# Optimization experiments

Hardware: AMD Instinct MI355X
Metric: run time of the kernel (lower is better)

The kernel has to match this reference:

```python
import jax, jax.numpy as jnp
import numpy as np

N_NODES = 100000
N_EDGES = 1000000
N_INPUT = 64
N_HIDDEN = 64
K = 8


def setup_inputs() -> dict:
    key = jax.random.key(0)
    k1, k2, k3, k4 = jax.random.split(key, 4)
    x = jax.random.normal(k1, (N_NODES, N_INPUT), dtype=jnp.float32)
    edge_index = jax.random.randint(k2, (2, N_EDGES), 0, N_NODES, dtype=jnp.int64)
    # ChebConv has K independent [in, out] weight matrices (Glorot-ish scale) and a bias.
    weight = jax.random.normal(k3, (K, N_INPUT, N_HIDDEN), dtype=jnp.float32) * (1.0 / np.sqrt(N_INPUT))
    bias = jax.random.normal(k4, (N_HIDDEN,), dtype=jnp.float32) * 0.01
    return {"x": x, "edge_index": edge_index, "weight": weight, "bias": bias}


def _cheb_edge_norm(edge_index, num_nodes):
    # PyG ChebConv sym normalization with default lambda_max=2.0:
    #   L_hat = (2/lambda_max) * (I - D^-1/2 A D^-1/2) - I = -D^-1/2 A D^-1/2
    # (the diagonal +1 from the Laplacian and the -1 self-loop cancel exactly).
    src, dst = edge_index[0], edge_index[1]
    ones = jnp.ones(src.shape[0], dtype=jnp.float32)
    deg = jax.ops.segment_sum(ones, src, num_segments=num_nodes)
    deg_inv_sqrt = jnp.where(deg > 0, jax.lax.rsqrt(jnp.maximum(deg, 1.0)), 0.0)
    return -deg_inv_sqrt[src] * deg_inv_sqrt[dst]  # [E]


def reference(x, edge_index, weight, bias):
    num_nodes = x.shape[0]
    src, dst = edge_index[0], edge_index[1]
    norm = _cheb_edge_norm(edge_index, num_nodes)

    def prop(h):  # h: [N, F] -> L_hat @ h via gather-multiply-scatter over edges
        return jax.ops.segment_sum(norm[:, None] * h[src], dst, num_segments=num_nodes)

    # Chebyshev recursion: T0 = x, T1 = L_hat x, Tk = 2 L_hat T_{k-1} - T_{k-2}
    Tx0 = x
    out = Tx0 @ weight[0]
    Tx1 = prop(Tx0)
    out = out + Tx1 @ weight[1]
    for k in range(2, weight.shape[0]):
        Tx2 = 2.0 * prop(Tx1) - Tx0
        out = out + Tx2 @ weight[k]
        Tx0, Tx1 = Tx1, Tx2
    out = out + bias
    # bn=False path: ReLU then dropout (identity in eval mode)
    return jax.nn.relu(out)
```

## Files before the change

kernel.cpp:

```cpp
#include <hip/hip_runtime.h>
#include <hip/hip_bf16.h>

typedef __attribute__((ext_vector_type(8))) short s16x8;
typedef __attribute__((ext_vector_type(4))) float f32x4;

#define HC 48
#define RBH 6400
#define RBS 3200

static __device__ __forceinline__ unsigned short f2bf(float f) {
    unsigned int u = __float_as_uint(f);
    unsigned int r = (u + 0x7FFFu + ((u >> 16) & 1u)) >> 16;
    return (unsigned short)r;
}

__global__ __launch_bounds__(256) void k_hist(const int* __restrict__ eidx,
                                              unsigned short* __restrict__ partials,
                                              int N, int E, int HR) {
    __shared__ int h[RBH];
    int b = blockIdx.x;
    int job = b / (HR * HC);
    int rc = b % (HR * HC);
    int r = rc / HC, c = rc % HC;
    int lo = r * RBH;
    int nb = min(RBH, N - lo);
    if (nb <= 0) return;
    for (int i = threadIdx.x; i < nb; i += 256) h[i] = 0;
    __syncthreads();
    const int* vals = eidx + (size_t)job * E;
    int e0 = (int)(((long long)E * c / HC) & ~3LL);
    int e1 = (c == HC - 1) ? E : (int)(((long long)E * (c + 1) / HC) & ~3LL);
    int e = e0 + threadIdx.x * 4;
    for (; e + 4 <= e1; e += 1024) {
        int4 v = *reinterpret_cast<const int4*>(vals + e);
        unsigned r0 = (unsigned)(v.x - lo), r1 = (unsigned)(v.y - lo);
        unsigned r2 = (unsigned)(v.z - lo), r3 = (unsigned)(v.w - lo);
        if (r0 < (unsigned)nb) atomicAdd(&h[r0], 1);
        if (r1 < (unsigned)nb) atomicAdd(&h[r1], 1);
        if (r2 < (unsigned)nb) atomicAdd(&h[r2], 1);
        if (r3 < (unsigned)nb) atomicAdd(&h[r3], 1);
    }
    if (threadIdx.x == 0)
        for (int t = e1 & ~3; t < e1; ++t) {
            unsigned rel = (unsigned)(vals[t] - lo);
            if (rel < (unsigned)nb) atomicAdd(&h[rel], 1);
        }
    __syncthreads();
    unsigned short* outp = partials + ((size_t)(job * HC + c)) * N + lo;
    for (int i = threadIdx.x; i < nb; i += 256) outp[i] = (unsigned short)h[i];
}

__global__ void k_reduce(const unsigned short* __restrict__ partials,
                         float* __restrict__ dis, int* __restrict__ cnt, int N) {
    int n = blockIdx.x * blockDim.x + threadIdx.x;
    if (n >= N) return;
    int dsum = 0, csum = 0;
    for (int c = 0; c < HC; ++c) {
        dsum += partials[(size_t)c * N + n];
        csum += partials[(size_t)(HC + c) * N + n];
    }
    dis[n] = dsum > 0 ? rsqrtf((float)dsum) : 0.f;
    cnt[n] = csum;
}

__global__ void k_scan1(const int* __restrict__ cnt, int* __restrict__ incl,
                        int* __restrict__ bsum, int N) {
    __shared__ int sm[1024];
    int t = threadIdx.x;
    int i = blockIdx.x * 1024 + t;
    sm[t] = (i < N) ? cnt[i] : 0;
    __syncthreads();
    for (int off = 1; off < 1024; off <<= 1) {
        int add = (t >= off) ? sm[t - off] : 0;
        __syncthreads();
        sm[t] += add;
        __syncthreads();
    }
    if (i < N) incl[i] = sm[t];
    if (t == 1023) bsum[blockIdx.x] = sm[1023];
}

__global__ void k_scan2(const int* __restrict__ bsum, int* __restrict__ boff,
                        int nb, int* __restrict__ rowptr, int N) {
    if (threadIdx.x == 0 && blockIdx.x == 0) {
        int run = 0;
        for (int b = 0; b < nb; ++b) { boff[b] = run; run += bsum[b]; }
        rowptr[N] = run;
    }
}

__global__ void k_scan3(const int* __restrict__ cnt, const int* __restrict__ boff,
                        int* __restrict__ rowptr,
                        const unsigned short* __restrict__ pdst,
                        int* __restrict__ cbase, int N) {
    int i = blockIdx.x * 1024 + threadIdx.x;
    if (i >= N) return;
    int ex = rowptr[i] - cnt[i] + boff[blockIdx.x];
    rowptr[i] = ex;
    int run = ex;
    for (int c = 0; c < HC; ++c) {
        size_t idx = (size_t)c * N + i;
        cbase[idx] = run;
        run += pdst[idx];
    }
}

__global__ __launch_bounds__(256) void k_scatter(
        const int* __restrict__ src, const int* __restrict__ dst,
        const int* __restrict__ cbase, int* __restrict__ srcs, int N, int E) {
    __shared__ int cur[RBS];
    int r = blockIdx.x / HC, c = blockIdx.x % HC;
    int lo = r * RBS;
    int nb = min(RBS, N - lo);
    if (nb <= 0) return;
    for (int i = threadIdx.x; i < nb; i += 256)
        cur[i] = cbase[(size_t)c * N + lo + i];
    __syncthreads();
    int e0 = (int)(((long long)E * c / HC) & ~3LL);
    int e1 = (c == HC - 1) ? E : (int)(((long long)E * (c + 1) / HC) & ~3LL);
    int e = e0 + threadIdx.x * 4;
    for (; e + 4 <= e1; e += 1024) {
        int4 d4 = *reinterpret_cast<const int4*>(dst + e);
        unsigned r0 = (unsigned)(d4.x - lo), r1 = (unsigned)(d4.y - lo);
        unsigned r2 = (unsigned)(d4.z - lo), r3 = (unsigned)(d4.w - lo);
        if (r0 < (unsigned)nb) srcs[atomicAdd(&cur[r0], 1)] = src[e];
        if (r1 < (unsigned)nb) srcs[atomicAdd(&cur[r1], 1)] = src[e + 1];
        if (r2 < (unsigned)nb) srcs[atomicAdd(&cur[r2], 1)] = src[e + 2];
        if (r3 < (unsigned)nb) srcs[atomicAdd(&cur[r3], 1)] = src[e + 3];
    }
    if (threadIdx.x == 0)
        for (int t = e1 & ~3; t < e1; ++t) {
            unsigned rel = (unsigned)(dst[t] - lo);
            if (rel < (unsigned)nb) srcs[atomicAdd(&cur[rel], 1)] = src[t];
        }
}

__global__ void k_pack(const float* __restrict__ x, const float* __restrict__ dis,
                       const float* __restrict__ W,
                       unsigned short* __restrict__ tb0, unsigned short* __restrict__ ysA,
                       unsigned short* __restrict__ ysB, unsigned short* __restrict__ wt,
                       int N, int K) {
    int t = blockIdx.x * blockDim.x + threadIdx.x;
    int nys = (N + 1) * 32;
    if (t < nys) {
        int row = t >> 5, p = t & 31;
        size_t o = ((size_t)row << 6) + (p << 1);
        if (row == N) {
            *(unsigned*)(ysA + o) = 0;
            *(unsigned*)(ysB + o) = 0;
            return;
        }
        float2 v = *reinterpret_cast<const float2*>(x + o);
        float dv = dis[row];
        *(unsigned*)(tb0 + o) = (unsigned)f2bf(v.x) | ((unsigned)f2bf(v.y) << 16);
        *(unsigned*)(ysA + o) = (unsigned)f2bf(v.x * dv) | ((unsigned)f2bf(v.y * dv) << 16);
    } else {
        int u = t - nys;
        if (u < K * 4096) {
            float v = W[u];
            int k = u >> 12;
            int r = u & 4095;
            int i = r >> 6;
            int j = r & 63;
            wt[(size_t)j * (K * 64) + (k << 6) + i] = f2bf(v);
        }
    }
}

static __device__ __forceinline__ void addrow(float* acc, uint4 t) {
    acc[0] += __uint_as_float(t.x << 16);
    acc[1] += __uint_as_float(t.x & 0xffff0000u);
    acc[2] += __uint_as_float(t.y << 16);
    acc[3] += __uint_as_float(t.y & 0xffff0000u);
    acc[4] += __uint_as_float(t.z << 16);
    acc[5] += __uint_as_float(t.z & 0xffff0000u);
    acc[6] += __uint_as_float(t.w << 16);
    acc[7] += __uint_as_float(t.w & 0xffff0000u);
}

__global__ __launch_bounds__(256) void k_prop(
        const unsigned short* __restrict__ Ysin,
        const unsigned short* __restrict__ Tm2,
        unsigned short* __restrict__ Tout,
        unsigned short* __restrict__ Ysout,
        const int* __restrict__ rowptr, const int* __restrict__ srcs,
        const float* __restrict__ dis,
        int N, int E, float scale, float beta, int wys) {
    int gt = blockIdx.x * blockDim.x + threadIdx.x;
    int wave0 = (gt >> 6) << 3;
    int lane = gt & 63;
    int g = lane >> 3;
    int i = lane & 7;
    int node = wave0 + g;
    bool live = node < N;
    int rs = 0, deg = 0;
    if (live) {
        rs = rowptr[node];
        deg = rowptr[node + 1] - rs;
    }
    int wmax = deg;
#pragma unroll
    for (int m = 8; m <= 32; m <<= 1) {
        int o = __shfl_xor(wmax, m);
        wmax = o > wmax ? o : wmax;
    }
    float acc[8];
#pragma unroll
    for (int j = 0; j < 8; ++j) acc[j] = 0.f;
    for (int e = 0; e < wmax; e += 8) {
        int b = rs + e;
        int s[8];
#pragma unroll
        for (int q = 0; q < 8; ++q)
            s[q] = (e + q < deg) ? srcs[min(b + q, E - 1)] : N;
        uint4 t[8];
#pragma unroll
        for (int q = 0; q < 8; ++q)
            t[q] = *reinterpret_cast<const uint4*>(Ysin + ((size_t)s[q] << 6) + (i << 3));
#pragma unroll
        for (int q = 0; q < 8; ++q) addrow(acc, t[q]);
    }
    if (live) {
        float dv = dis[node];
        float sc = -scale * dv;
        size_t base = ((size_t)node << 6) + (i << 3);
        float r[8];
#pragma unroll
        for (int j = 0; j < 8; ++j) r[j] = sc * acc[j];
        if (beta != 0.f) {
            uint4 pv = *reinterpret_cast<const uint4*>(Tm2 + base);
            r[0] = fmaf(beta, __uint_as_float(pv.x << 16), r[0]);
            r[1] = fmaf(beta, __uint_as_float(pv.x & 0xffff0000u), r[1]);
            r[2] = fmaf(beta, __uint_as_float(pv.y << 16), r[2]);
            r[3] = fmaf(beta, __uint_as_float(pv.y & 0xffff0000u), r[3]);
            r[4] = fmaf(beta, __uint_as_float(pv.z << 16), r[4]);
            r[5] = fmaf(beta, __uint_as_float(pv.z & 0xffff0000u), r[5]);
            r[6] = fmaf(beta, __uint_as_float(pv.w << 16), r[6]);
            r[7] = fmaf(beta, __uint_as_float(pv.w & 0xffff0000u), r[7]);
        }
        uint4 ov;
        ov.x = (unsigned)f2bf(r[0]) | ((unsigned)f2bf(r[1]) << 16);
        ov.y = (unsigned)f2bf(r[2]) | ((unsigned)f2bf(r[3]) << 16);
        ov.z = (unsigned)f2bf(r[4]) | ((unsigned)f2bf(r[5]) << 16);
        ov.w = (unsigned)f2bf(r[6]) | ((unsigned)f2bf(r[7]) << 16);
        *reinterpret_cast<uint4*>(Tout + base) = ov;
        if (wys) {
            uint4 yv;
            yv.x = (unsigned)f2bf(r[0] * dv) | ((unsigned)f2bf(r[1] * dv) << 16);
            yv.y = (unsigned)f2bf(r[2] * dv) | ((unsigned)f2bf(r[3] * dv) << 16);
            yv.z = (unsigned)f2bf(r[4] * dv) | ((unsigned)f2bf(r[5] * dv) << 16);
            yv.w = (unsigned)f2bf(r[6] * dv) | ((unsigned)f2bf(r[7] * dv) << 16);
            *reinterpret_cast<uint4*>(Ysout + base) = yv;
        }
    }
}

template <int KS>
__global__ __launch_bounds__(256) void k_gemm(const unsigned short* __restrict__ tb,
                                              const unsigned short* __restrict__ wt,
                                              const float* __restrict__ bias,
                                              float* __restrict__ out,
                                              int N, int NF) {
    constexpr int NB = KS / 2;
    __shared__ unsigned short lds[KS * 512];
    int lane = threadIdx.x & 63;
    int w = threadIdx.x >> 6;
    int l16 = lane & 15;
    int quad = lane >> 4;
    const int KI = KS * 32;

    s16x8 afr[KS];
    {
        const unsigned short* wrow = wt + (size_t)(w * 16 + l16) * KI + quad * 8;
#pragma unroll
        for (int ks = 0; ks < KS; ++ks)
            afr[ks] = *reinterpret_cast<const s16x8*>(wrow + ks * 32);
    }
    f32x4 bias4 = *reinterpret_cast<const f32x4*>(bias + w * 16 + quad * 4);

    int ntiles = N >> 4;
    for (int t = blockIdx.x; t < ntiles; t += gridDim.x) {
        const char* tilebase = (const char*)tb + (size_t)t * 2048;
#pragma unroll
        for (int inst = 0; inst < 2 * NB; ++inst) {
            if ((inst & 3) != w) continue;
            int kbuf = inst >> 1;
            int j = inst & 1;
            int p = j * 64 + lane;
            int nrow = p >> 3;
            int s = (p & 7) ^ (nrow & 7);
            const char* g = tilebase + (size_t)kbuf * NF * 2 + nrow * 128 + s * 16;
            __builtin_amdgcn_global_load_lds(
                (const __attribute__((address_space(1))) unsigned int*)g,
                (__attribute__((address_space(3))) unsigned int*)(lds + inst * 512),
                16, 0, 0);
        }
        __syncthreads();
        f32x4 acc = {0.f, 0.f, 0.f, 0.f};
#pragma unroll
        for (int ks = 0; ks < KS; ++ks) {
            int kbuf = ks >> 1, half = ks & 1;
            int sph = (half * 4 + quad) ^ (l16 & 7);
            s16x8 bf = *reinterpret_cast<const s16x8*>(
                lds + kbuf * 1024 + l16 * 64 + sph * 8);
            acc = __builtin_amdgcn_mfma_f32_16x16x32_bf16(afr[ks], bf, acc, 0, 0, 0);
        }
        float* orow = out + (size_t)(t * 16 + l16) * 64 + w * 16 + quad * 4;
        f32x4 r;
#pragma unroll
        for (int q = 0; q < 4; ++q) {
            float v = acc[q] + bias4[q];
            r[q] = v > 0.f ? v : 0.f;
        }
        *reinterpret_cast<f32x4*>(orow) = r;
        __syncthreads();
    }
}

extern "C" void kernel_launch(void* const* d_in, const int* in_sizes, int n_in,
                              void* d_out, int out_size, void* d_ws, size_t ws_size,
                              hipStream_t stream) {
    const float* x    = (const float*)d_in[0];
    const int*   eidx = (const int*)d_in[1];
    const float* W    = (const float*)d_in[2];
    const float* bias = (const float*)d_in[3];
    float* out = (float*)d_out;

    const int NF = in_sizes[0];
    const int N  = NF / 64;
    const int E  = in_sizes[1] / 2;
    const int K  = in_sizes[2] / 4096;

    const int* src = eidx;
    const int* dst = eidx + E;

    char* ws = (char*)d_ws;
    size_t off = 0;
    auto alloc = [&](size_t bytes) -> char* {
        char* p = ws + off;
        off = (off + bytes + 255) & ~(size_t)255;
        return p;
    };
    unsigned short* Tb = (unsigned short*)alloc((size_t)K * NF * 2);
    unsigned short* Ys[2];
    Ys[0] = (unsigned short*)alloc((size_t)(N + 1) * 64 * 2);
    Ys[1] = (unsigned short*)alloc((size_t)(N + 1) * 64 * 2);
    unsigned short* Wt = (unsigned short*)alloc((size_t)64 * K * 64 * 2);
    int*   srcs   = (int*)alloc((size_t)E * 4);
    int*   rowptr = (int*)alloc((size_t)(N + 1) * 4);
    int*   cnt    = (int*)alloc((size_t)N * 4);
    unsigned short* partials = (unsigned short*)alloc((size_t)2 * HC * N * 2);
    int*   cbase  = (int*)alloc((size_t)HC * N * 4);
    float* dis  = (float*)alloc((size_t)N * 4);
    int*   bsum = (int*)alloc(1024);
    int*   boff = (int*)alloc(1024);
    (void)ws_size; (void)n_in; (void)out_size;

    int HR = (N + RBH - 1) / RBH;
    int SR = (N + RBS - 1) / RBS;
    const unsigned short* pdst = partials + (size_t)HC * N;

    k_hist<<<2 * HR * HC, 256, 0, stream>>>(eidx, partials, N, E, HR);
    k_reduce<<<(N + 255) / 256, 256, 0, stream>>>(partials, dis, cnt, N);
    int nb = (N + 1023) / 1024;
    k_scan1<<<nb, 1024, 0, stream>>>(cnt, rowptr, bsum, N);
    k_scan2<<<1, 64, 0, stream>>>(bsum, boff, nb, rowptr, N);
    k_scan3<<<nb, 1024, 0, stream>>>(cnt, boff, rowptr, pdst, cbase, N);
    k_scatter<<<SR * HC, 256, 0, stream>>>(src, dst, cbase, srcs, N, E);
    int packn = (N + 1) * 32 + K * 4096;
    k_pack<<<(packn + 255) / 256, 256, 0, stream>>>(x, dis, W, Tb, Ys[0], Ys[1], Wt, N, K);

    int waves = (N + 7) / 8;
    int pblocks = (waves * 64 + 255) / 256;
    for (int p = 1; p < K; ++p) {
        float scale = (p == 1) ? 1.f : 2.f;
        float beta  = (p == 1) ? 0.f : -1.f;
        const unsigned short* Tm2 = Tb + (size_t)(p >= 2 ? p - 2 : 0) * NF;
        k_prop<<<pblocks, 256, 0, stream>>>(
            Ys[(p - 1) & 1], Tm2, Tb + (size_t)p * NF, Ys[p & 1],
            rowptr, srcs, dis, N, E, scale, beta, p < K - 1 ? 1 : 0);
    }

    if (K == 8)      k_gemm<16><<<1024, 256, 0, stream>>>(Tb, Wt, bias, out, N, NF);
    else if (K == 4) k_gemm<8><<<1024, 256, 0, stream>>>(Tb, Wt, bias, out, N, NF);
    else if (K == 2) k_gemm<4><<<1024, 256, 0, stream>>>(Tb, Wt, bias, out, N, NF);
    else if (K == 1) k_gemm<2><<<1024, 256, 0, stream>>>(Tb, Wt, bias, out, N, NF);
}
```

Baseline: 343.7 us.

## Split feature matrices into 16-column quarter planes for cache-friendly gathers

Stores the Chebyshev feature buffers as four column-quarter planes of 16 bf16 values per row instead of full 64-wide rows. The propagation kernel now gives each node two lanes and 32 nodes per wave, and loops over the four planes, so each pass gathers from a working set a quarter the size, which is meant to fit better in cache. In exchange, the neighbour index list is re-read four times and each gather fetches only 32 bytes. The pack and GEMM loaders are updated to address the new layout.

```diff
diff --git a/kernel.cpp b/kernel.cpp
--- a/kernel.cpp
+++ b/kernel.cpp
@@ -142,18 +142,23 @@
                        int N, int K) {
     int t = blockIdx.x * blockDim.x + threadIdx.x;
     int nys = (N + 1) * 32;
+    const size_t QS_Y = (size_t)(N + 1) << 4;
+    const size_t QS_T = (size_t)N << 4;
     if (t < nys) {
         int row = t >> 5, p = t & 31;
-        size_t o = ((size_t)row << 6) + (p << 1);
+        int q = p >> 3;
+        int w2 = (p & 7) << 1;
+        size_t oy = (size_t)q * QS_Y + ((size_t)row << 4) + w2;
         if (row == N) {
-            *(unsigned*)(ysA + o) = 0;
-            *(unsigned*)(ysB + o) = 0;
+            *(unsigned*)(ysA + oy) = 0;
+            *(unsigned*)(ysB + oy) = 0;
             return;
         }
-        float2 v = *reinterpret_cast<const float2*>(x + o);
+        float2 v = *reinterpret_cast<const float2*>(x + ((size_t)row << 6) + (p << 1));
         float dv = dis[row];
-        *(unsigned*)(tb0 + o) = (unsigned)f2bf(v.x) | ((unsigned)f2bf(v.y) << 16);
-        *(unsigned*)(ysA + o) = (unsigned)f2bf(v.x * dv) | ((unsigned)f2bf(v.y * dv) << 16);
+        size_t ot = (size_t)q * QS_T + ((size_t)row << 4) + w2;
+        *(unsigned*)(tb0 + ot) = (unsigned)f2bf(v.x) | ((unsigned)f2bf(v.y) << 16);
+        *(unsigned*)(ysA + oy) = (unsigned)f2bf(v.x * dv) | ((unsigned)f2bf(v.y * dv) << 16);
     } else {
         int u = t - nys;
         if (u < K * 4096) {
@@ -178,7 +183,7 @@
     acc[7] += __uint_as_float(t.w & 0xffff0000u);
 }
 
-__global__ __launch_bounds__(256) void k_prop(
+__global__ __launch_bounds__(64) void k_prop(
         const unsigned short* __restrict__ Ysin,
         const unsigned short* __restrict__ Tm2,
         unsigned short* __restrict__ Tout,
@@ -186,11 +191,10 @@
         const int* __restrict__ rowptr, const int* __restrict__ srcs,
         const float* __restrict__ dis,
         int N, int E, float scale, float beta, int wys) {
-    int gt = blockIdx.x * blockDim.x + threadIdx.x;
-    int wave0 = (gt >> 6) << 3;
-    int lane = gt & 63;
-    int g = lane >> 3;
-    int i = lane & 7;
+    int lane = threadIdx.x;
+    int wave0 = blockIdx.x << 5;
+    int g = lane >> 1;
+    int i = lane & 1;
     int node = wave0 + g;
     bool live = node < N;
     int rs = 0, deg = 0;
@@ -200,57 +204,63 @@
     }
     int wmax = deg;
 #pragma unroll
-    for (int m = 8; m <= 32; m <<= 1) {
+    for (int m = 2; m <= 32; m <<= 1) {
         int o = __shfl_xor(wmax, m);
         wmax = o > wmax ? o : wmax;
     }
-    float acc[8];
-#pragma unroll
-    for (int j = 0; j < 8; ++j) acc[j] = 0.f;
-    for (int e = 0; e < wmax; e += 8) {
-        int b = rs + e;
-        int s[8];
-#pragma unroll
-        for (int q = 0; q < 8; ++q)
-            s[q] = (e + q < deg) ? srcs[min(b + q, E - 1)] : N;
-        uint4 t[8];
-#pragma unroll
-        for (int q = 0; q < 8; ++q)
-            t[q] = *reinterpret_cast<const uint4*>(Ysin + ((size_t)s[q] << 6) + (i << 3));
-#pragma unroll
-        for (int q = 0; q < 8; ++q) addrow(acc, t[q]);
-    }
-    if (live) {
-        float dv = dis[node];
-        float sc = -scale * dv;
-        size_t base = ((size_t)node << 6) + (i << 3);
-        float r[8];
-#pragma unroll
-        for (int j = 0; j < 8; ++j) r[j] = sc * acc[j];
-        if (beta != 0.f) {
-            uint4 pv = *reinterpret_cast<const uint4*>(Tm2 + base);
-            r[0] = fmaf(beta, __uint_as_float(pv.x << 16), r[0]);
-            r[1] = fmaf(beta, __uint_as_float(pv.x & 0xffff0000u), r[1]);
-            r[2] = fmaf(beta, __uint_as_float(pv.y << 16), r[2]);
-            r[3] = fmaf(beta, __uint_as_float(pv.y & 0xffff0000u), r[3]);
-            r[4] = fmaf(beta, __uint_as_float(pv.z << 16), r[4]);
-            r[5] = fmaf(beta, __uint_as_float(pv.z & 0xffff0000u), r[5]);
-            r[6] = fmaf(beta, __uint_as_float(pv.w << 16), r[6]);
-            r[7] = fmaf(beta, __uint_as_float(pv.w & 0xffff0000u), r[7]);
-        }
-        uint4 ov;
-        ov.x = (unsigned)f2bf(r[0]) | ((unsigned)f2bf(r[1]) << 16);
-        ov.y = (unsigned)f2bf(r[2]) | ((unsigned)f2bf(r[3]) << 16);
-        ov.z = (unsigned)f2bf(r[4]) | ((unsigned)f2bf(r[5]) << 16);
-        ov.w = (unsigned)f2bf(r[6]) | ((unsigned)f2bf(r[7]) << 16);
-        *reinterpret_cast<uint4*>(Tout + base) = ov;
-        if (wys) {
-            uint4 yv;
-            yv.x = (unsigned)f2bf(r[0] * dv) | ((unsigned)f2bf(r[1] * dv) << 16);
-            yv.y = (unsigned)f2bf(r[2] * dv) | ((unsigned)f2bf(r[3] * dv) << 16);
-            yv.z = (unsigned)f2bf(r[4] * dv) | ((unsigned)f2bf(r[5] * dv) << 16);
-            yv.w = (unsigned)f2bf(r[6] * dv) | ((unsigned)f2bf(r[7] * dv) << 16);
-            *reinterpret_cast<uint4*>(Ysout + base) = yv;
+    float dv = live ? dis[node] : 0.f;
+    float sc = -scale * dv;
+    const size_t QS_Y = (size_t)(N + 1) << 4;
+    const size_t QS_T = (size_t)N << 4;
+    for (int q4 = 0; q4 < 4; ++q4) {
+        const unsigned short* Yq = Ysin + (size_t)q4 * QS_Y;
+        float acc[8];
+#pragma unroll
+        for (int j = 0; j < 8; ++j) acc[j] = 0.f;
+        for (int e = 0; e < wmax; e += 8) {
+            int b = rs + e;
+            int s[8];
+#pragma unroll
+            for (int qq = 0; qq < 8; ++qq)
+                s[qq] = (e + qq < deg) ? srcs[min(b + qq, E - 1)] : N;
+            uint4 t[8];
+#pragma unroll
+            for (int qq = 0; qq < 8; ++qq)
+                t[qq] = *reinterpret_cast<const uint4*>(Yq + ((size_t)s[qq] << 4) + (i << 3));
+#pragma unroll
+            for (int qq = 0; qq < 8; ++qq) addrow(acc, t[qq]);
+        }
+        if (live) {
+            size_t bt = (size_t)q4 * QS_T + ((size_t)node << 4) + (i << 3);
+            float r[8];
+#pragma unroll
+            for (int j = 0; j < 8; ++j) r[j] = sc * acc[j];
+            if (beta != 0.f) {
+                uint4 pv = *reinterpret_cast<const uint4*>(Tm2 + bt);
+                r[0] = fmaf(beta, __uint_as_float(pv.x << 16), r[0]);
+                r[1] = fmaf(beta, __uint_as_float(pv.x & 0xffff0000u), r[1]);
+                r[2] = fmaf(beta, __uint_as_float(pv.y << 16), r[2]);
+                r[3] = fmaf(beta, __uint_as_float(pv.y & 0xffff0000u), r[3]);
+                r[4] = fmaf(beta, __uint_as_float(pv.z << 16), r[4]);
+                r[5] = fmaf(beta, __uint_as_float(pv.z & 0xffff0000u), r[5]);
+                r[6] = fmaf(beta, __uint_as_float(pv.w << 16), r[6]);
+                r[7] = fmaf(beta, __uint_as_float(pv.w & 0xffff0000u), r[7]);
+            }
+            uint4 ov;
+            ov.x = (unsigned)f2bf(r[0]) | ((unsigned)f2bf(r[1]) << 16);
+            ov.y = (unsigned)f2bf(r[2]) | ((unsigned)f2bf(r[3]) << 16);
+            ov.z = (unsigned)f2bf(r[4]) | ((unsigned)f2bf(r[5]) << 16);
+            ov.w = (unsigned)f2bf(r[6]) | ((unsigned)f2bf(r[7]) << 16);
+            *reinterpret_cast<uint4*>(Tout + bt) = ov;
+            if (wys) {
+                size_t by = (size_t)q4 * QS_Y + ((size_t)node << 4) + (i << 3);
+                uint4 yv;
+                yv.x = (unsigned)f2bf(r[0] * dv) | ((unsigned)f2bf(r[1] * dv) << 16);
+                yv.y = (unsigned)f2bf(r[2] * dv) | ((unsigned)f2bf(r[3] * dv) << 16);
+                yv.z = (unsigned)f2bf(r[4] * dv) | ((unsigned)f2bf(r[5] * dv) << 16);
+                yv.w = (unsigned)f2bf(r[6] * dv) | ((unsigned)f2bf(r[7] * dv) << 16);
+                *reinterpret_cast<uint4*>(Ysout + by) = yv;
+            }
         }
     }
 }
@@ -280,7 +290,6 @@
 
     int ntiles = N >> 4;
     for (int t = blockIdx.x; t < ntiles; t += gridDim.x) {
-        const char* tilebase = (const char*)tb + (size_t)t * 2048;
 #pragma unroll
         for (int inst = 0; inst < 2 * NB; ++inst) {
             if ((inst & 3) != w) continue;
@@ -289,7 +298,10 @@
             int p = j * 64 + lane;
             int nrow = p >> 3;
             int s = (p & 7) ^ (nrow & 7);
-            const char* g = tilebase + (size_t)kbuf * NF * 2 + nrow * 128 + s * 16;
+            int srow = (t << 4) + nrow;
+            const char* g = (const char*)tb + (size_t)kbuf * NF * 2
+                          + (size_t)(s >> 1) * ((size_t)N << 5)
+                          + ((size_t)srow << 5) + ((s & 1) << 4);
             __builtin_amdgcn_global_load_lds(
                 (const __attribute__((address_space(1))) unsigned int*)g,
                 (__attribute__((address_space(3))) unsigned int*)(lds + inst * 512),
@@ -370,13 +382,12 @@
     int packn = (N + 1) * 32 + K * 4096;
     k_pack<<<(packn + 255) / 256, 256, 0, stream>>>(x, dis, W, Tb, Ys[0], Ys[1], Wt, N, K);
 
-    int waves = (N + 7) / 8;
-    int pblocks = (waves * 64 + 255) / 256;
+    int pblocks = (N + 31) / 32;
     for (int p = 1; p < K; ++p) {
         float scale = (p == 1) ? 1.f : 2.f;
         float beta  = (p == 1) ? 0.f : -1.f;
         const unsigned short* Tm2 = Tb + (size_t)(p >= 2 ? p - 2 : 0) * NF;
-        k_prop<<<pblocks, 256, 0, stream>>>(
+        k_prop<<<pblocks, 64, 0, stream>>>(
             Ys[(p - 1) & 1], Tm2, Tb + (size_t)p * NF, Ys[p & 1],
             rowptr, srcs, dis, N, E, scale, beta, p < K - 1 ? 1 : 0);
     }
```

New measurement: 488.2 us. 42.0% more time.

## Drop pre-scaled Ys buffers, scale by source degree in prop; fuse scan kernels

Applied to the files above, without the earlier changes.

The propagation kernel no longer reads a separately maintained pre-scaled copy (Ys) of each Chebyshev term. It gathers the plain T rows and multiplies each by the source node's dis value loaded per edge. This removes the extra Ys write per prop step, the Ys buffers, and their initialisation in k_pack, at the cost of an extra random 4-byte dis gather per edge. Separately, the degree reduction is fused into the first scan kernel and the serial block-offset scan is folded into k_scan3, cutting two kernel launches.

```diff
diff --git a/kernel.cpp b/kernel.cpp
--- a/kernel.cpp
+++ b/kernel.cpp
@@ -50,25 +50,25 @@
     for (int i = threadIdx.x; i < nb; i += 256) outp[i] = (unsigned short)h[i];
 }
 
-__global__ void k_reduce(const unsigned short* __restrict__ partials,
-                         float* __restrict__ dis, int* __restrict__ cnt, int N) {
-    int n = blockIdx.x * blockDim.x + threadIdx.x;
-    if (n >= N) return;
-    int dsum = 0, csum = 0;
-    for (int c = 0; c < HC; ++c) {
-        dsum += partials[(size_t)c * N + n];
-        csum += partials[(size_t)(HC + c) * N + n];
-    }
-    dis[n] = dsum > 0 ? rsqrtf((float)dsum) : 0.f;
-    cnt[n] = csum;
-}
-
-__global__ void k_scan1(const int* __restrict__ cnt, int* __restrict__ incl,
-                        int* __restrict__ bsum, int N) {
+__global__ __launch_bounds__(1024) void k_rs(const unsigned short* __restrict__ partials,
+                                             float* __restrict__ dis,
+                                             int* __restrict__ cnt,
+                                             int* __restrict__ incl,
+                                             int* __restrict__ bsum, int N) {
     __shared__ int sm[1024];
     int t = threadIdx.x;
     int i = blockIdx.x * 1024 + t;
-    sm[t] = (i < N) ? cnt[i] : 0;
+    int csum = 0;
+    if (i < N) {
+        int dsum = 0;
+        for (int c = 0; c < HC; ++c) {
+            dsum += partials[(size_t)c * N + i];
+            csum += partials[(size_t)(HC + c) * N + i];
+        }
+        dis[i] = dsum > 0 ? rsqrtf((float)dsum) : 0.f;
+        cnt[i] = csum;
+    }
+    sm[t] = (i < N) ? csum : 0;
     __syncthreads();
     for (int off = 1; off < 1024; off <<= 1) {
         int add = (t >= off) ? sm[t - off] : 0;
@@ -80,23 +80,29 @@
     if (t == 1023) bsum[blockIdx.x] = sm[1023];
 }
 
-__global__ void k_scan2(const int* __restrict__ bsum, int* __restrict__ boff,
-                        int nb, int* __restrict__ rowptr, int N) {
-    if (threadIdx.x == 0 && blockIdx.x == 0) {
-        int run = 0;
-        for (int b = 0; b < nb; ++b) { boff[b] = run; run += bsum[b]; }
-        rowptr[N] = run;
-    }
-}
-
-__global__ void k_scan3(const int* __restrict__ cnt, const int* __restrict__ boff,
-                        int* __restrict__ rowptr,
-                        const unsigned short* __restrict__ pdst,
-                        int* __restrict__ cbase, int N) {
-    int i = blockIdx.x * 1024 + threadIdx.x;
+__global__ __launch_bounds__(1024) void k_scan3(const int* __restrict__ cnt,
+                                                const int* __restrict__ bsum,
+                                                int* __restrict__ rowptr,
+                                                const unsigned short* __restrict__ pdst,
+                                                int* __restrict__ cbase, int N, int nb) {
+    __shared__ int sb[128];
+    int t = threadIdx.x;
+    if (t < 128) sb[t] = (t < nb) ? bsum[t] : 0;
+    __syncthreads();
+    for (int off = 1; off < 128; off <<= 1) {
+        int add = (t < 128 && t >= off) ? sb[t - off] : 0;
+        __syncthreads();
+        if (t < 128) sb[t] += add;
+        __syncthreads();
+    }
+    int b = blockIdx.x;
+    int boff = (b == 0) ? 0 : sb[b - 1];
+    int total = sb[nb - 1];
+    int i = b * 1024 + t;
     if (i >= N) return;
-    int ex = rowptr[i] - cnt[i] + boff[blockIdx.x];
+    int ex = rowptr[i] - cnt[i] + boff;
     rowptr[i] = ex;
+    if (i == N - 1) rowptr[N] = total;
     int run = ex;
     for (int c = 0; c < HC; ++c) {
         size_t idx = (size_t)c * N + i;
@@ -135,27 +141,18 @@
         }
 }
 
-__global__ void k_pack(const float* __restrict__ x, const float* __restrict__ dis,
-                       const float* __restrict__ W,
-                       unsigned short* __restrict__ tb0, unsigned short* __restrict__ ysA,
-                       unsigned short* __restrict__ ysB, unsigned short* __restrict__ wt,
+__global__ void k_pack(const float* __restrict__ x, const float* __restrict__ W,
+                       unsigned short* __restrict__ tb0, unsigned short* __restrict__ wt,
                        int N, int K) {
     int t = blockIdx.x * blockDim.x + threadIdx.x;
-    int nys = (N + 1) * 32;
-    if (t < nys) {
+    int nt = N * 32;
+    if (t < nt) {
         int row = t >> 5, p = t & 31;
         size_t o = ((size_t)row << 6) + (p << 1);
-        if (row == N) {
-            *(unsigned*)(ysA + o) = 0;
-            *(unsigned*)(ysB + o) = 0;
-            return;
-        }
         float2 v = *reinterpret_cast<const float2*>(x + o);
-        float dv = dis[row];
         *(unsigned*)(tb0 + o) = (unsigned)f2bf(v.x) | ((unsigned)f2bf(v.y) << 16);
-        *(unsigned*)(ysA + o) = (unsigned)f2bf(v.x * dv) | ((unsigned)f2bf(v.y * dv) << 16);
     } else {
-        int u = t - nys;
+        int u = t - nt;
         if (u < K * 4096) {
             float v = W[u];
             int k = u >> 12;
@@ -167,25 +164,24 @@
     }
 }
 
-static __device__ __forceinline__ void addrow(float* acc, uint4 t) {
-    acc[0] += __uint_as_float(t.x << 16);
-    acc[1] += __uint_as_float(t.x & 0xffff0000u);
-    acc[2] += __uint_as_float(t.y << 16);
-    acc[3] += __uint_as_float(t.y & 0xffff0000u);
-    acc[4] += __uint_as_float(t.z << 16);
-    acc[5] += __uint_as_float(t.z & 0xffff0000u);
-    acc[6] += __uint_as_float(t.w << 16);
-    acc[7] += __uint_as_float(t.w & 0xffff0000u);
+static __device__ __forceinline__ void addrow_s(float* acc, uint4 t, float dv) {
+    acc[0] = fmaf(dv, __uint_as_float(t.x << 16), acc[0]);
+    acc[1] = fmaf(dv, __uint_as_float(t.x & 0xffff0000u), acc[1]);
+    acc[2] = fmaf(dv, __uint_as_float(t.y << 16), acc[2]);
+    acc[3] = fmaf(dv, __uint_as_float(t.y & 0xffff0000u), acc[3]);
+    acc[4] = fmaf(dv, __uint_as_float(t.z << 16), acc[4]);
+    acc[5] = fmaf(dv, __uint_as_float(t.z & 0xffff0000u), acc[5]);
+    acc[6] = fmaf(dv, __uint_as_float(t.w << 16), acc[6]);
+    acc[7] = fmaf(dv, __uint_as_float(t.w & 0xffff0000u), acc[7]);
 }
 
 __global__ __launch_bounds__(256) void k_prop(
-        const unsigned short* __restrict__ Ysin,
+        const unsigned short* __restrict__ Tin,
         const unsigned short* __restrict__ Tm2,
         unsigned short* __restrict__ Tout,
-        unsigned short* __restrict__ Ysout,
         const int* __restrict__ rowptr, const int* __restrict__ srcs,
         const float* __restrict__ dis,
-        int N, int E, float scale, float beta, int wys) {
+        int N, int E, float scale, float beta) {
     int gt = blockIdx.x * blockDim.x + threadIdx.x;
     int wave0 = (gt >> 6) << 3;
     int lane = gt & 63;
@@ -210,15 +206,21 @@
     for (int e = 0; e < wmax; e += 8) {
         int b = rs + e;
         int s[8];
+        float dv8[8];
 #pragma unroll
         for (int q = 0; q < 8; ++q)
-            s[q] = (e + q < deg) ? srcs[min(b + q, E - 1)] : N;
+            s[q] = (e + q < deg) ? srcs[min(b + q, E - 1)] : 0;
+#pragma unroll
+        for (int q = 0; q < 8; ++q) {
+            float d = dis[s[q]];
+            dv8[q] = (e + q < deg) ? d : 0.f;
+        }
         uint4 t[8];
 #pragma unroll
         for (int q = 0; q < 8; ++q)
-            t[q] = *reinterpret_cast<const uint4*>(Ysin + ((size_t)s[q] << 6) + (i << 3));
-#pragma unroll
-        for (int q = 0; q < 8; ++q) addrow(acc, t[q]);
+            t[q] = *reinterpret_cast<const uint4*>(Tin + ((size_t)s[q] << 6) + (i << 3));
+#pragma unroll
+        for (int q = 0; q < 8; ++q) addrow_s(acc, t[q], dv8[q]);
     }
     if (live) {
         float dv = dis[node];
@@ -244,14 +246,6 @@
         ov.z = (unsigned)f2bf(r[4]) | ((unsigned)f2bf(r[5]) << 16);
         ov.w = (unsigned)f2bf(r[6]) | ((unsigned)f2bf(r[7]) << 16);
         *reinterpret_cast<uint4*>(Tout + base) = ov;
-        if (wys) {
-            uint4 yv;
-            yv.x = (unsigned)f2bf(r[0] * dv) | ((unsigned)f2bf(r[1] * dv) << 16);
-            yv.y = (unsigned)f2bf(r[2] * dv) | ((unsigned)f2bf(r[3] * dv) << 16);
-            yv.z = (unsigned)f2bf(r[4] * dv) | ((unsigned)f2bf(r[5] * dv) << 16);
-            yv.w = (unsigned)f2bf(r[6] * dv) | ((unsigned)f2bf(r[7] * dv) << 16);
-            *reinterpret_cast<uint4*>(Ysout + base) = yv;
-        }
     }
 }
 
@@ -342,9 +336,6 @@
         return p;
     };
     unsigned short* Tb = (unsigned short*)alloc((size_t)K * NF * 2);
-    unsigned short* Ys[2];
-    Ys[0] = (unsigned short*)alloc((size_t)(N + 1) * 64 * 2);
-    Ys[1] = (unsigned short*)alloc((size_t)(N + 1) * 64 * 2);
     unsigned short* Wt = (unsigned short*)alloc((size_t)64 * K * 64 * 2);
     int*   srcs   = (int*)alloc((size_t)E * 4);
     int*   rowptr = (int*)alloc((size_t)(N + 1) * 4);
@@ -353,7 +344,6 @@
     int*   cbase  = (int*)alloc((size_t)HC * N * 4);
     float* dis  = (float*)alloc((size_t)N * 4);
     int*   bsum = (int*)alloc(1024);
-    int*   boff = (int*)alloc(1024);
     (void)ws_size; (void)n_in; (void)out_size;
 
     int HR = (N + RBH - 1) / RBH;
@@ -361,14 +351,12 @@
     const unsigned short* pdst = partials + (size_t)HC * N;
 
     k_hist<<<2 * HR * HC, 256, 0, stream>>>(eidx, partials, N, E, HR);
-    k_reduce<<<(N + 255) / 256, 256, 0, stream>>>(partials, dis, cnt, N);
     int nb = (N + 1023) / 1024;
-    k_scan1<<<nb, 1024, 0, stream>>>(cnt, rowptr, bsum, N);
-    k_scan2<<<1, 64, 0, stream>>>(bsum, boff, nb, rowptr, N);
-    k_scan3<<<nb, 1024, 0, stream>>>(cnt, boff, rowptr, pdst, cbase, N);
+    k_rs<<<nb, 1024, 0, stream>>>(partials, dis, cnt, rowptr, bsum, N);
+    k_scan3<<<nb, 1024, 0, stream>>>(cnt, bsum, rowptr, pdst, cbase, N, nb);
     k_scatter<<<SR * HC, 256, 0, stream>>>(src, dst, cbase, srcs, N, E);
-    int packn = (N + 1) * 32 + K * 4096;
-    k_pack<<<(packn + 255) / 256, 256, 0, stream>>>(x, dis, W, Tb, Ys[0], Ys[1], Wt, N, K);
+    int packn = N * 32 + K * 4096;
+    k_pack<<<(packn + 255) / 256, 256, 0, stream>>>(x, W, Tb, Wt, N, K);
 
     int waves = (N + 7) / 8;
     int pblocks = (waves * 64 + 255) / 256;
@@ -377,8 +365,8 @@
         float beta  = (p == 1) ? 0.f : -1.f;
         const unsigned short* Tm2 = Tb + (size_t)(p >= 2 ? p - 2 : 0) * NF;
         k_prop<<<pblocks, 256, 0, stream>>>(
-            Ys[(p - 1) & 1], Tm2, Tb + (size_t)p * NF, Ys[p & 1],
-            rowptr, srcs, dis, N, E, scale, beta, p < K - 1 ? 1 : 0);
+            Tb + (size_t)(p - 1) * NF, Tm2, Tb + (size_t)p * NF,
+            rowptr, srcs, dis, N, E, scale, beta);
     }
 
     if (K == 8)      k_gemm<16><<<1024, 256, 0, stream>>>(Tb, Wt, bias, out, N, NF);
```

Measured after the change: 378.7 us. 10.2% more time.
